# Performance work log

Hardware: AMD Instinct MI355X
Metric: run time of the kernel (lower is better)

Reference implementation:

```python
import jax, jax.numpy as jnp
import numpy as np

K_SAMPLE = 64
ALPHA = 1.0  # SmoothTop1SVM margin
TAU = 1.0    # SmoothTop1SVM temperature
NEG_INF = -1e30


def smooth_top1_svm(logits, y):
    # logits: [n, 2], y: [n] int. Smooth top-1 SVM loss (mean over instances).
    x_y = jnp.take_along_axis(logits, y[:, None], axis=1)[:, 0]          # [n]
    delta = ALPHA * (1.0 - jax.nn.one_hot(y, logits.shape[1], dtype=logits.dtype))
    z = (logits + delta - x_y[:, None]) / TAU                             # [n, 2]
    return TAU * jnp.mean(jax.nn.logsumexp(z, axis=1))


def setup_inputs() -> dict:
    key = jax.random.key(0)
    ks = jax.random.split(key, 10)
    B, N, D, A = 8, 16384, 1024, 128
    X = jax.random.normal(ks[0], (B, N, D), dtype=jnp.float32)
    mask = jnp.ones((B, N), dtype=jnp.float32)
    labels = jax.random.randint(ks[1], (B,), 0, 2)
    # AttentionPool params: fc1 (D->A), tanh, fc2 (A->1)
    W1 = jax.random.normal(ks[2], (D, A), dtype=jnp.float32) / np.sqrt(D)
    b1 = jnp.zeros((A,), dtype=jnp.float32)
    w2 = jax.random.normal(ks[3], (A,), dtype=jnp.float32) / np.sqrt(A)
    b2 = jnp.zeros((), dtype=jnp.float32)
    # Bag classifier (D->1)
    Wc = jax.random.normal(ks[4], (D, 1), dtype=jnp.float32) / np.sqrt(D)
    bc = jnp.zeros((1,), dtype=jnp.float32)
    # Two instance classifiers (D->2), stacked
    Wi = jax.random.normal(ks[5], (2, D, 2), dtype=jnp.float32) / np.sqrt(D)
    bi = jnp.zeros((2, 2), dtype=jnp.float32)
    return {"X": X, "mask": mask, "labels": labels, "W1": W1, "b1": b1,
            "w2": w2, "b2": b2, "Wc": Wc, "bc": bc, "Wi": Wi, "bi": bi}


def _clam_loss(X, mask, labels, W1, b1, w2, b2, Wc, bc, Wi, bi):
    # Attention pool: f = w2^T tanh(X W1 + b1) + b2  (pre-softmax attention)
    h = jnp.tanh(jnp.einsum('bnd,da->bna', X, W1) + b1)
    f = jnp.einsum('bna,a->bn', h, w2) + b2                               # [B, N]
    s = jax.nn.softmax(jnp.where(mask > 0, f, NEG_INF), axis=1)           # [B, N]
    z = jnp.einsum('bn,bnd->bd', s, X)                                    # [B, D]
    bag_pred = z @ Wc[:, 0] + bc[0]                                       # [B]

    labels_f = labels.astype(bag_pred.dtype)
    # BCEWithLogitsLoss (mean): softplus(x) - x*y, numerically stable
    crit_loss = jnp.mean(jax.nn.softplus(bag_pred) - bag_pred * labels_f)

    k = K_SAMPLE
    pos_t = jnp.ones((k,), dtype=jnp.int32)
    neg_t = jnp.zeros((k,), dtype=jnp.int32)
    in_targets = jnp.concatenate([pos_t, neg_t])                          # [2k]

    def per_bag(att_i, emb_i, label):
        # in-class branch uses classifier[label]; out-of-class uses classifier[1-label]
        Win, bin_ = Wi[label], bi[label]
        Wout, bout = Wi[1 - label], bi[1 - label]
        _, top_p_ids = jax.lax.top_k(att_i, k)
        _, top_n_ids = jax.lax.top_k(-att_i, k)
        top_p = emb_i[top_p_ids]                                          # [k, D]
        top_n = emb_i[top_n_ids]                                          # [k, D]
        inst = jnp.concatenate([top_p, top_n], axis=0)                    # [2k, D]
        logits_in = inst @ Win + bin_                                     # [2k, 2]
        loss_in = smooth_top1_svm(logits_in, in_targets)
        logits_out = top_p @ Wout + bout                                  # [k, 2]
        loss_out = smooth_top1_svm(logits_out, neg_t)
        return loss_in + loss_out

    inst_loss = jnp.sum(jax.vmap(per_bag)(f, X, labels))
    # Concatenate outputs into one vector: [bag_pred (B), crit_loss, inst_loss]
    return jnp.concatenate([bag_pred, crit_loss[None], inst_loss[None]])


def reference(X, mask, labels, W1, b1, w2, b2, Wc, bc, Wi, bi):
    return _clam_loss(X, mask, labels, W1, b1, w2, b2, Wc, bc, Wi, bi)
```

## Files before the change

kernel.cpp:

```cpp
#include <hip/hip_runtime.h>
#include <hip/hip_bf16.h>

#define BB 8
#define NN 16384
#define DD 1024
#define AA 128

typedef __attribute__((ext_vector_type(8))) short bf16x8;
typedef __attribute__((ext_vector_type(4))) float f32x4;
typedef __attribute__((ext_vector_type(4))) unsigned short u16x4;

__device__ __forceinline__ unsigned short f2bf(float x) {
  union { __hip_bfloat16 h; unsigned short u; } cv;
  cv.h = __float2bfloat16(x);
  return cv.u;
}

__device__ __forceinline__ float softplusf(float x) {
  return fmaxf(x, 0.f) + log1pf(expf(-fabsf(x)));
}

__device__ __forceinline__ unsigned int ordu(float x) {
  unsigned int u = __float_as_uint(x);
  return (u & 0x80000000u) ? ~u : (u | 0x80000000u);
}

__device__ __forceinline__ int fvx(int i) {
  return i ^ ((i >> 6) & 63);
}

__device__ __forceinline__ void gload16(const void* g, void* l) {
  __builtin_amdgcn_global_load_lds(
      (const __attribute__((address_space(1))) unsigned int*)g,
      (__attribute__((address_space(3))) unsigned int*)l, 16, 0, 0);
}

__global__ __launch_bounds__(256) void k_prep(
    const float* __restrict__ W1, unsigned short* __restrict__ W1Ts,
    float* __restrict__ out) {
  const int gid = blockIdx.x * 256 + threadIdx.x;
  if (gid == 0) { out[8] = 0.f; out[9] = 0.f; }
  if (gid < DD * AA) {
    const int k = gid >> 7, col = gid & 127;
    const int kp = k >> 6, kin = k & 63;
    const int g = kin >> 3, j = kin & 7;
    W1Ts[kp * 8192 + col * 64 + ((g ^ (col & 7)) << 3) + j] =
        f2bf(W1[k * AA + col]);
  }
}

__global__ __launch_bounds__(256) void k_scores(
    const float* __restrict__ X, const unsigned short* __restrict__ W1Ts,
    const float* __restrict__ b1, const float* __restrict__ w2,
    const float* __restrict__ b2p, const float* __restrict__ Wc,
    float* __restrict__ f, float* __restrict__ y) {
  __shared__ unsigned short As[128 * 64];
  __shared__ unsigned short Bs[128 * 64];
  __shared__ float fpart[128];
  const int t = threadIdx.x;
  const int lane = t & 63;
  const int wv = t >> 6;
  const int wr = wv >> 1, wc = wv & 1;
  const int l15 = lane & 15, lg = lane >> 4;
  const size_t row0 = (size_t)blockIdx.x * 128;
  const float* Xb = X + row0 * DD;

  f32x4 zero4 = {0.f, 0.f, 0.f, 0.f};
  f32x4 acc[4][4];
#pragma unroll
  for (int mi = 0; mi < 4; ++mi)
#pragma unroll
    for (int ni = 0; ni < 4; ++ni) acc[mi][ni] = zero4;

  float yp[8];
#pragma unroll
  for (int j = 0; j < 8; ++j) yp[j] = 0.f;

  for (int st = 0; st < 16; ++st) {
    const int k0 = st * 64;
    {
      const unsigned short* Pp = W1Ts + st * 8192;
#pragma unroll
      for (int q = 0; q < 4; ++q)
        gload16(Pp + ((wv * 4 + q) * 64 + lane) * 8,
                &Bs[((wv * 4 + q) * 64 + lane) * 8]);
    }
    const int kq = (t & 15) * 4;
    const float4 wc4 = *(const float4*)(Wc + k0 + kq);
#pragma unroll
    for (int j = 0; j < 8; ++j) {
      const int i = t + j * 256;
      const int r = i >> 4;
      float4 v = *(const float4*)(Xb + (size_t)r * DD + k0 + kq);
      yp[j] += v.x * wc4.x + v.y * wc4.y + v.z * wc4.z + v.w * wc4.w;
      u16x4 p;
      p.x = f2bf(v.x); p.y = f2bf(v.y); p.z = f2bf(v.z); p.w = f2bf(v.w);
      const int idx = r * 64 + (((kq >> 3) ^ (r & 7)) << 3) + (kq & 7);
      *(u16x4*)&As[idx] = p;
    }
    __syncthreads();
#pragma unroll
    for (int ks = 0; ks < 2; ++ks) {
      bf16x8 af[4], bg[4];
      const int chunk = ks * 4 + lg;
#pragma unroll
      for (int mi = 0; mi < 4; ++mi) {
        const int r = wr * 64 + mi * 16 + l15;
        af[mi] = *(const bf16x8*)&As[r * 64 + ((chunk ^ (r & 7)) << 3)];
      }
#pragma unroll
      for (int ni = 0; ni < 4; ++ni) {
        const int c = wc * 64 + ni * 16 + l15;
        bg[ni] = *(const bf16x8*)&Bs[c * 64 + ((chunk ^ (c & 7)) << 3)];
      }
#pragma unroll
      for (int mi = 0; mi < 4; ++mi)
#pragma unroll
        for (int ni = 0; ni < 4; ++ni)
          acc[mi][ni] = __builtin_amdgcn_mfma_f32_16x16x32_bf16(
              af[mi], bg[ni], acc[mi][ni], 0, 0, 0);
    }
    __syncthreads();
  }

#pragma unroll
  for (int j = 0; j < 8; ++j) {
    float s = yp[j];
    s += __shfl_xor(s, 1);
    s += __shfl_xor(s, 2);
    s += __shfl_xor(s, 4);
    s += __shfl_xor(s, 8);
    if ((t & 15) == 0) y[row0 + (t >> 4) + j * 16] = s;
  }

  const float b2 = b2p[0];
  float w2c[4], b1c[4];
#pragma unroll
  for (int ni = 0; ni < 4; ++ni) {
    const int c = wc * 64 + ni * 16 + l15;
    w2c[ni] = w2[c];
    b1c[ni] = b1[c];
  }
  float pr[4][4];
#pragma unroll
  for (int mi = 0; mi < 4; ++mi) {
#pragma unroll
    for (int q = 0; q < 4; ++q) {
      float s = 0.f;
#pragma unroll
      for (int ni = 0; ni < 4; ++ni)
        s += w2c[ni] * tanhf(acc[mi][ni][q] + b1c[ni]);
      s += __shfl_xor(s, 1);
      s += __shfl_xor(s, 2);
      s += __shfl_xor(s, 4);
      s += __shfl_xor(s, 8);
      pr[mi][q] = s;
    }
  }
  if (wc == 1 && l15 == 0) {
#pragma unroll
    for (int mi = 0; mi < 4; ++mi)
#pragma unroll
      for (int q = 0; q < 4; ++q)
        fpart[wr * 64 + mi * 16 + lg * 4 + q] = pr[mi][q];
  }
  __syncthreads();
  if (wc == 0 && l15 == 0) {
#pragma unroll
    for (int mi = 0; mi < 4; ++mi)
#pragma unroll
      for (int q = 0; q < 4; ++q) {
        const int rl = wr * 64 + mi * 16 + lg * 4 + q;
        f[row0 + rl] = pr[mi][q] + fpart[rl] + b2;
      }
  }
}

__global__ __launch_bounds__(1024) void k_select(
    const float* __restrict__ f, const float* __restrict__ y,
    const float* __restrict__ mask, const int* __restrict__ labels,
    const float* __restrict__ bc, int* __restrict__ sel,
    float* __restrict__ out) {
  __shared__ unsigned int uv[NN];
  __shared__ unsigned int whist[16][256];
  __shared__ unsigned int wq[4];
  __shared__ unsigned int sb[4];
  __shared__ float redf[16];
  const int t = threadIdx.x;
  const int lane = t & 63, w = t >> 6;
  const int b = blockIdx.x >> 1;
  const int mode = blockIdx.x & 1;
  const float* fb = f + (size_t)b * NN;
  const float* yb = y + (size_t)b * NN;
  const float* kb = mask + (size_t)b * NN;

  if (mode == 0) {
    float mx = -3.0e38f;
    for (int i = t; i < NN; i += 1024) {
      const float v = fb[i];
      uv[fvx(i)] = ordu(v);
      mx = fmaxf(mx, kb[i] > 0.f ? v : -1.0e30f);
    }
#pragma unroll
    for (int s = 1; s < 64; s <<= 1) mx = fmaxf(mx, __shfl_xor(mx, s));
    if (lane == 0) redf[w] = mx;
    __syncthreads();
    float m = redf[0];
#pragma unroll
    for (int q = 1; q < 16; ++q) m = fmaxf(m, redf[q]);
    __syncthreads();

    float se = 0.f, sy = 0.f;
    for (int i = t; i < NN; i += 1024) {
      if (kb[i] > 0.f) {
        const float e = expf(fb[i] - m);
        se += e;
        sy += e * yb[i];
      }
    }
#pragma unroll
    for (int s = 1; s < 64; s <<= 1) se += __shfl_xor(se, s);
    if (lane == 0) redf[w] = se;
    __syncthreads();
    float Z = 0.f;
#pragma unroll
    for (int q = 0; q < 16; ++q) Z += redf[q];
    __syncthreads();
#pragma unroll
    for (int s = 1; s < 64; s <<= 1) sy += __shfl_xor(sy, s);
    if (lane == 0) redf[w] = sy;
    __syncthreads();
    if (t == 0) {
      float Sy = 0.f;
#pragma unroll
      for (int q = 0; q < 16; ++q) Sy += redf[q];
      const float bp = Sy / Z + bc[0];
      out[b] = bp;
      const float lf = (float)labels[b];
      atomicAdd(out + 8, (softplusf(bp) - bp * lf) * 0.125f);
    }
  } else {
    for (int i = t; i < NN; i += 1024) uv[fvx(i)] = ~ordu(fb[i]);
  }
  __syncthreads();

  const int i0 = t * 16;
  unsigned int pref = 0u, above = 0u, krem = 64u;
  for (int p = 3; p >= 0; --p) {
    for (int q = t; q < 4096; q += 1024) ((unsigned int*)whist)[q] = 0u;
    __syncthreads();
    const unsigned int pmask = (p == 3) ? 0u : (0xFFFFFFFFu << ((p + 1) * 8));
    for (int j = 0; j < 16; ++j) {
      const unsigned int u = uv[fvx(i0 + j)];
      if ((u & pmask) == pref)
        atomicAdd(&whist[w][(u >> (p * 8)) & 255u], 1u);
    }
    __syncthreads();
    unsigned int v = 0, s = 0;
    if (t < 256) {
#pragma unroll
      for (int q = 0; q < 16; ++q) v += whist[q][t];
      s = v;
#pragma unroll
      for (int off = 1; off < 64; off <<= 1) {
        const unsigned int o = __shfl_down(s, off);
        if (lane + off < 64) s += o;
      }
      if (lane == 0) wq[w] = s;
    }
    __syncthreads();
    if (t < 256) {
      unsigned int hi = 0;
      for (int q = w + 1; q < 4; ++q) hi += wq[q];
      const unsigned int Ssuf = s + hi;
      const unsigned int Snext = Ssuf - v;
      if (Ssuf >= krem && Snext < krem) {
        sb[0] = pref | ((unsigned int)t << (p * 8));
        sb[1] = above + Snext;
        sb[2] = krem - Snext;
        sb[3] = 0u;
      }
    }
    __syncthreads();
    pref = sb[0]; above = sb[1]; krem = sb[2];
  }
  const int off = b * 128 + mode * 64;
  unsigned int myt = 0;
  for (int j = 0; j < 16; ++j) {
    const unsigned int u = uv[fvx(i0 + j)];
    if (u > pref) {
      const unsigned int pos = atomicAdd(&sb[3], 1u);
      sel[off + pos] = i0 + j;
    } else if (u == pref) {
      myt++;
    }
  }
  unsigned int pv = myt;
#pragma unroll
  for (int o2 = 1; o2 < 64; o2 <<= 1) {
    const unsigned int o = __shfl_up(pv, o2);
    if (lane >= o2) pv += o;
  }
  __syncthreads();
  if (lane == 63) ((unsigned int*)whist)[w] = pv;
  __syncthreads();
  unsigned int base = 0;
  for (int q = 0; q < w; ++q) base += ((unsigned int*)whist)[q];
  unsigned int gg = base + pv - myt;
  for (int j = 0; j < 16 && myt > 0; ++j) {
    const unsigned int u = uv[fvx(i0 + j)];
    if (u == pref) {
      if (gg < krem) sel[off + above + gg] = i0 + j;
      gg++;
      myt--;
    }
  }
}

__global__ __launch_bounds__(256) void k_final(
    const float* __restrict__ X, const int* __restrict__ labels,
    const int* __restrict__ sel, const float* __restrict__ Wi,
    const float* __restrict__ bi, float* __restrict__ out) {
  const int b = blockIdx.x >> 2, part = blockIdx.x & 3;
  const int t = threadIdx.x;
  const int lane = t & 63, w = t >> 6;
  __shared__ float sin_[4], sout_[4];
  const int label = labels[b];

  const float* Win = Wi + label * (DD * 2);
  const float* Wot = Wi + (1 - label) * (DD * 2);
  const float bin0 = bi[label * 2], bin1 = bi[label * 2 + 1];
  const float bo0 = bi[(1 - label) * 2], bo1 = bi[(1 - label) * 2 + 1];
  float ain = 0.f, aout = 0.f;
  for (int ii = 0; ii < 8; ++ii) {
    const int r = part * 32 + w * 8 + ii;
    const int id = sel[b * 128 + r];
    const float* xr = X + ((size_t)b * NN + id) * DD;
    float p0 = 0.f, p1 = 0.f, p2 = 0.f, p3 = 0.f;
#pragma unroll
    for (int j = 0; j < 16; j += 4) {
      const int d = lane * 16 + j;
      const float4 x = *(const float4*)(xr + d);
      const float4 wa = *(const float4*)(Win + d * 2);
      const float4 wb = *(const float4*)(Win + d * 2 + 4);
      p0 += x.x * wa.x + x.y * wa.z + x.z * wb.x + x.w * wb.z;
      p1 += x.x * wa.y + x.y * wa.w + x.z * wb.y + x.w * wb.w;
      if (r < 64) {
        const float4 oa = *(const float4*)(Wot + d * 2);
        const float4 ob = *(const float4*)(Wot + d * 2 + 4);
        p2 += x.x * oa.x + x.y * oa.z + x.z * ob.x + x.w * ob.z;
        p3 += x.x * oa.y + x.y * oa.w + x.z * ob.y + x.w * ob.w;
      }
    }
#pragma unroll
    for (int sh = 1; sh < 64; sh <<= 1) {
      p0 += __shfl_xor(p0, sh);
      p1 += __shfl_xor(p1, sh);
      p2 += __shfl_xor(p2, sh);
      p3 += __shfl_xor(p3, sh);
    }
    if (lane == 0) {
      const float l0 = p0 + bin0, l1 = p1 + bin1;
      ain += (r < 64) ? softplusf(l0 + 1.f - l1) : softplusf(l1 + 1.f - l0);
      if (r < 64) aout += softplusf((p3 + bo1) + 1.f - (p2 + bo0));
    }
  }
  if (lane == 0) { sin_[w] = ain; sout_[w] = aout; }
  __syncthreads();
  if (t == 0) {
    const float ti = sin_[0] + sin_[1] + sin_[2] + sin_[3];
    const float to = sout_[0] + sout_[1] + sout_[2] + sout_[3];
    atomicAdd(out + 9, ti * (1.0f / 128.0f) + to * (1.0f / 64.0f));
  }
}


extern "C" void kernel_launch(void* const* d_in, const int* in_sizes, int n_in,
                              void* d_out, int out_size, void* d_ws, size_t ws_size,
                              hipStream_t stream) {
  const float* X      = (const float*)d_in[0];
  const float* mask   = (const float*)d_in[1];
  const int*   labels = (const int*)d_in[2];
  const float* W1     = (const float*)d_in[3];
  const float* b1     = (const float*)d_in[4];
  const float* w2     = (const float*)d_in[5];
  const float* b2     = (const float*)d_in[6];
  const float* Wc     = (const float*)d_in[7];
  const float* bc     = (const float*)d_in[8];
  const float* Wi     = (const float*)d_in[9];
  const float* bi     = (const float*)d_in[10];
  float* out = (float*)d_out;

  float* ws  = (float*)d_ws;
  float* f   = ws;
  float* y   = ws + 131072;
  int*   sel = (int*)(ws + 262144);
  unsigned short* W1Ts = (unsigned short*)(ws + 263168);

  k_prep  <<<512,  256, 0, stream>>>(W1, W1Ts, out);
  k_scores<<<1024, 256, 0, stream>>>(X, W1Ts, b1, w2, b2, Wc, f, y);
  k_select<<<16,  1024, 0, stream>>>(f, y, mask, labels, bc, sel, out);
  k_final <<<32,   256, 0, stream>>>(X, labels, sel, Wi, bi, out);
}
```

Baseline: 207.1 us.

## Halve score tile rows to 64 and fuse instance loss into select kernel

The score GEMM now uses 64-row tiles, with each wave owning 16 rows across all 128 attention columns. This doubles the grid to 2048 blocks, shrinks shared memory and drops the cross-wave f reduction. The final instance-classifier kernel is folded into k_select, which keeps the selected indices in shared memory and computes the SVM losses directly, removing one launch and the global sel buffer. The cost is that the W1 B-tile is loaded from global memory twice as often overall, and the loss step now runs on only 16 blocks instead of 32.

```diff
diff --git a/kernel.cpp b/kernel.cpp
--- a/kernel.cpp
+++ b/kernel.cpp
@@ -5,6 +5,8 @@
 #define NN 16384
 #define DD 1024
 #define AA 128
+#define ROWS 64
+#define NBLKS (BB * NN / ROWS)
 
 typedef __attribute__((ext_vector_type(8))) short bf16x8;
 typedef __attribute__((ext_vector_type(4))) float f32x4;
@@ -54,27 +56,23 @@
     const float* __restrict__ b1, const float* __restrict__ w2,
     const float* __restrict__ b2p, const float* __restrict__ Wc,
     float* __restrict__ f, float* __restrict__ y) {
-  __shared__ unsigned short As[128 * 64];
+  __shared__ unsigned short As[ROWS * 64];
   __shared__ unsigned short Bs[128 * 64];
-  __shared__ float fpart[128];
   const int t = threadIdx.x;
   const int lane = t & 63;
   const int wv = t >> 6;
-  const int wr = wv >> 1, wc = wv & 1;
   const int l15 = lane & 15, lg = lane >> 4;
-  const size_t row0 = (size_t)blockIdx.x * 128;
+  const size_t row0 = (size_t)blockIdx.x * ROWS;
   const float* Xb = X + row0 * DD;
 
   f32x4 zero4 = {0.f, 0.f, 0.f, 0.f};
-  f32x4 acc[4][4];
-#pragma unroll
-  for (int mi = 0; mi < 4; ++mi)
-#pragma unroll
-    for (int ni = 0; ni < 4; ++ni) acc[mi][ni] = zero4;
-
-  float yp[8];
-#pragma unroll
-  for (int j = 0; j < 8; ++j) yp[j] = 0.f;
+  f32x4 acc[8];
+#pragma unroll
+  for (int ni = 0; ni < 8; ++ni) acc[ni] = zero4;
+
+  float yp[4];
+#pragma unroll
+  for (int j = 0; j < 4; ++j) yp[j] = 0.f;
 
   for (int st = 0; st < 16; ++st) {
     const int k0 = st * 64;
@@ -88,7 +86,7 @@
     const int kq = (t & 15) * 4;
     const float4 wc4 = *(const float4*)(Wc + k0 + kq);
 #pragma unroll
-    for (int j = 0; j < 8; ++j) {
+    for (int j = 0; j < 4; ++j) {
       const int i = t + j * 256;
       const int r = i >> 4;
       float4 v = *(const float4*)(Xb + (size_t)r * DD + k0 + kq);
@@ -99,32 +97,25 @@
       *(u16x4*)&As[idx] = p;
     }
     __syncthreads();
+    const int r = wv * 16 + l15;
+    const int rx = r & 7;
 #pragma unroll
     for (int ks = 0; ks < 2; ++ks) {
-      bf16x8 af[4], bg[4];
       const int chunk = ks * 4 + lg;
-#pragma unroll
-      for (int mi = 0; mi < 4; ++mi) {
-        const int r = wr * 64 + mi * 16 + l15;
-        af[mi] = *(const bf16x8*)&As[r * 64 + ((chunk ^ (r & 7)) << 3)];
-      }
-#pragma unroll
-      for (int ni = 0; ni < 4; ++ni) {
-        const int c = wc * 64 + ni * 16 + l15;
-        bg[ni] = *(const bf16x8*)&Bs[c * 64 + ((chunk ^ (c & 7)) << 3)];
-      }
-#pragma unroll
-      for (int mi = 0; mi < 4; ++mi)
-#pragma unroll
-        for (int ni = 0; ni < 4; ++ni)
-          acc[mi][ni] = __builtin_amdgcn_mfma_f32_16x16x32_bf16(
-              af[mi], bg[ni], acc[mi][ni], 0, 0, 0);
-    }
-    __syncthreads();
-  }
-
-#pragma unroll
-  for (int j = 0; j < 8; ++j) {
+      const bf16x8 af = *(const bf16x8*)&As[r * 64 + ((chunk ^ rx) << 3)];
+#pragma unroll
+      for (int ni = 0; ni < 8; ++ni) {
+        const int c = ni * 16 + l15;
+        const bf16x8 bg =
+            *(const bf16x8*)&Bs[c * 64 + ((chunk ^ (c & 7)) << 3)];
+        acc[ni] = __builtin_amdgcn_mfma_f32_16x16x32_bf16(af, bg, acc[ni], 0, 0, 0);
+      }
+    }
+    __syncthreads();
+  }
+
+#pragma unroll
+  for (int j = 0; j < 4; ++j) {
     float s = yp[j];
     s += __shfl_xor(s, 1);
     s += __shfl_xor(s, 2);
@@ -134,58 +125,39 @@
   }
 
   const float b2 = b2p[0];
-  float w2c[4], b1c[4];
-#pragma unroll
-  for (int ni = 0; ni < 4; ++ni) {
-    const int c = wc * 64 + ni * 16 + l15;
-    w2c[ni] = w2[c];
-    b1c[ni] = b1[c];
-  }
-  float pr[4][4];
-#pragma unroll
-  for (int mi = 0; mi < 4; ++mi) {
-#pragma unroll
-    for (int q = 0; q < 4; ++q) {
-      float s = 0.f;
-#pragma unroll
-      for (int ni = 0; ni < 4; ++ni)
-        s += w2c[ni] * tanhf(acc[mi][ni][q] + b1c[ni]);
-      s += __shfl_xor(s, 1);
-      s += __shfl_xor(s, 2);
-      s += __shfl_xor(s, 4);
-      s += __shfl_xor(s, 8);
-      pr[mi][q] = s;
-    }
-  }
-  if (wc == 1 && l15 == 0) {
-#pragma unroll
-    for (int mi = 0; mi < 4; ++mi)
-#pragma unroll
-      for (int q = 0; q < 4; ++q)
-        fpart[wr * 64 + mi * 16 + lg * 4 + q] = pr[mi][q];
-  }
-  __syncthreads();
-  if (wc == 0 && l15 == 0) {
-#pragma unroll
-    for (int mi = 0; mi < 4; ++mi)
-#pragma unroll
-      for (int q = 0; q < 4; ++q) {
-        const int rl = wr * 64 + mi * 16 + lg * 4 + q;
-        f[row0 + rl] = pr[mi][q] + fpart[rl] + b2;
-      }
+  float w2c[8], b1c[8];
+#pragma unroll
+  for (int ni = 0; ni < 8; ++ni) {
+    w2c[ni] = w2[ni * 16 + l15];
+    b1c[ni] = b1[ni * 16 + l15];
+  }
+#pragma unroll
+  for (int q = 0; q < 4; ++q) {
+    float s = 0.f;
+#pragma unroll
+    for (int ni = 0; ni < 8; ++ni)
+      s += w2c[ni] * tanhf(acc[ni][q] + b1c[ni]);
+    s += __shfl_xor(s, 1);
+    s += __shfl_xor(s, 2);
+    s += __shfl_xor(s, 4);
+    s += __shfl_xor(s, 8);
+    if (l15 == 0) f[row0 + wv * 16 + lg * 4 + q] = s + b2;
   }
 }
 
 __global__ __launch_bounds__(1024) void k_select(
     const float* __restrict__ f, const float* __restrict__ y,
     const float* __restrict__ mask, const int* __restrict__ labels,
-    const float* __restrict__ bc, int* __restrict__ sel,
+    const float* __restrict__ bc, const float* __restrict__ X,
+    const float* __restrict__ Wi, const float* __restrict__ bi,
     float* __restrict__ out) {
   __shared__ unsigned int uv[NN];
   __shared__ unsigned int whist[16][256];
+  __shared__ unsigned int selL[64];
   __shared__ unsigned int wq[4];
   __shared__ unsigned int sb[4];
   __shared__ float redf[16];
+  __shared__ float redo[16];
   const int t = threadIdx.x;
   const int lane = t & 63, w = t >> 6;
   const int b = blockIdx.x >> 1;
@@ -284,13 +256,12 @@
     __syncthreads();
     pref = sb[0]; above = sb[1]; krem = sb[2];
   }
-  const int off = b * 128 + mode * 64;
   unsigned int myt = 0;
   for (int j = 0; j < 16; ++j) {
     const unsigned int u = uv[fvx(i0 + j)];
     if (u > pref) {
       const unsigned int pos = atomicAdd(&sb[3], 1u);
-      sel[off + pos] = i0 + j;
+      selL[pos] = i0 + j;
     } else if (u == pref) {
       myt++;
     }
@@ -310,31 +281,21 @@
   for (int j = 0; j < 16 && myt > 0; ++j) {
     const unsigned int u = uv[fvx(i0 + j)];
     if (u == pref) {
-      if (gg < krem) sel[off + above + gg] = i0 + j;
+      if (gg < krem) selL[above + gg] = i0 + j;
       gg++;
       myt--;
     }
   }
-}
-
-__global__ __launch_bounds__(256) void k_final(
-    const float* __restrict__ X, const int* __restrict__ labels,
-    const int* __restrict__ sel, const float* __restrict__ Wi,
-    const float* __restrict__ bi, float* __restrict__ out) {
-  const int b = blockIdx.x >> 2, part = blockIdx.x & 3;
-  const int t = threadIdx.x;
-  const int lane = t & 63, w = t >> 6;
-  __shared__ float sin_[4], sout_[4];
+  __syncthreads();
+
   const int label = labels[b];
-
   const float* Win = Wi + label * (DD * 2);
   const float* Wot = Wi + (1 - label) * (DD * 2);
   const float bin0 = bi[label * 2], bin1 = bi[label * 2 + 1];
   const float bo0 = bi[(1 - label) * 2], bo1 = bi[(1 - label) * 2 + 1];
   float ain = 0.f, aout = 0.f;
-  for (int ii = 0; ii < 8; ++ii) {
-    const int r = part * 32 + w * 8 + ii;
-    const int id = sel[b * 128 + r];
+  for (int rr = w; rr < 64; rr += 16) {
+    const int id = selL[rr];
     const float* xr = X + ((size_t)b * NN + id) * DD;
     float p0 = 0.f, p1 = 0.f, p2 = 0.f, p3 = 0.f;
 #pragma unroll
@@ -345,7 +306,7 @@
       const float4 wb = *(const float4*)(Win + d * 2 + 4);
       p0 += x.x * wa.x + x.y * wa.z + x.z * wb.x + x.w * wb.z;
       p1 += x.x * wa.y + x.y * wa.w + x.z * wb.y + x.w * wb.w;
-      if (r < 64) {
+      if (mode == 0) {
         const float4 oa = *(const float4*)(Wot + d * 2);
         const float4 ob = *(const float4*)(Wot + d * 2 + 4);
         p2 += x.x * oa.x + x.y * oa.z + x.z * ob.x + x.w * ob.z;
@@ -361,15 +322,20 @@
     }
     if (lane == 0) {
       const float l0 = p0 + bin0, l1 = p1 + bin1;
-      ain += (r < 64) ? softplusf(l0 + 1.f - l1) : softplusf(l1 + 1.f - l0);
-      if (r < 64) aout += softplusf((p3 + bo1) + 1.f - (p2 + bo0));
-    }
-  }
-  if (lane == 0) { sin_[w] = ain; sout_[w] = aout; }
+      if (mode == 0) {
+        ain += softplusf(l0 + 1.f - l1);
+        aout += softplusf((p3 + bo1) + 1.f - (p2 + bo0));
+      } else {
+        ain += softplusf(l1 + 1.f - l0);
+      }
+    }
+  }
+  if (lane == 0) { redf[w] = ain; redo[w] = aout; }
   __syncthreads();
   if (t == 0) {
-    const float ti = sin_[0] + sin_[1] + sin_[2] + sin_[3];
-    const float to = sout_[0] + sout_[1] + sout_[2] + sout_[3];
+    float ti = 0.f, to = 0.f;
+#pragma unroll
+    for (int q = 0; q < 16; ++q) { ti += redf[q]; to += redo[q]; }
     atomicAdd(out + 9, ti * (1.0f / 128.0f) + to * (1.0f / 64.0f));
   }
 }
@@ -394,11 +360,9 @@
   float* ws  = (float*)d_ws;
   float* f   = ws;
   float* y   = ws + 131072;
-  int*   sel = (int*)(ws + 262144);
-  unsigned short* W1Ts = (unsigned short*)(ws + 263168);
-
-  k_prep  <<<512,  256, 0, stream>>>(W1, W1Ts, out);
-  k_scores<<<1024, 256, 0, stream>>>(X, W1Ts, b1, w2, b2, Wc, f, y);
-  k_select<<<16,  1024, 0, stream>>>(f, y, mask, labels, bc, sel, out);
-  k_final <<<32,   256, 0, stream>>>(X, labels, sel, Wi, bi, out);
-}
+  unsigned short* W1Ts = (unsigned short*)(ws + 262144);
+
+  k_prep  <<<512,   256, 0, stream>>>(W1, W1Ts, out);
+  k_scores<<<NBLKS, 256, 0, stream>>>(X, W1Ts, b1, w2, b2, Wc, f, y);
+  k_select<<<16,   1024, 0, stream>>>(f, y, mask, labels, bc, X, Wi, bi, out);
+}
```

Result: faster. 182.1 us (-12.1%).
